# Kernel optimization log

Measured on AMD Instinct MI355X. Metric: run time of the kernel, lower is better.

Reference implementation:

```python
import jax, jax.numpy as jnp
import numpy as np

B, N, IN_DIM, OUT_DIM = 8, 2048, 128, 128
NEG_SLOPE = 0.2

def setup_inputs() -> dict:
    key = jax.random.key(0)
    k1, k2, k3, k4 = jax.random.split(key, 4)
    x = jax.random.normal(k1, (B, N, IN_DIM), dtype=jnp.float32)
    adj = jax.random.randint(k2, (N, N), 0, 2, dtype=jnp.int32)
    # nn.Linear weight init scale ~ 1/sqrt(fan_in)
    W = jax.random.normal(k3, (IN_DIM, OUT_DIM), dtype=jnp.float32) / np.sqrt(IN_DIM)
    a_vec = jax.random.normal(k4, (2 * OUT_DIM,), dtype=jnp.float32) / np.sqrt(2 * OUT_DIM)
    return {"x": x, "adj": adj, "W": W, "a_vec": a_vec}

def reference(x, adj, W, a_vec):
    # h = x @ W : [b, n, d]
    h = jnp.einsum("bni,io->bno", x, W)
    # Algebraic decomposition of a([h_i, h_j]) = a1.h_i + a2.h_j
    a1, a2 = a_vec[:OUT_DIM], a_vec[OUT_DIM:]
    s_i = h @ a1  # [b, n] score contribution from source node i
    s_j = h @ a2  # [b, n] score contribution from target node j
    e = s_i[:, :, None] + s_j[:, None, :]  # [b, n, n]
    e = jnp.where(e >= 0, e, NEG_SLOPE * e)  # leaky_relu(0.2)
    mask = (adj > 0)[None, :, :]  # [1, n, n] broadcast over batch
    e = jnp.where(mask, e, -jnp.inf)
    alpha = jax.nn.softmax(e, axis=-1)  # [b, n, n]
    out = jnp.einsum("bnm,bmd->bnd", alpha, h)  # [b, n, d]
    return out, alpha
```

## Files before the change

kernel.cpp:

```cpp
#include <hip/hip_runtime.h>
#include <hip/hip_bf16.h>
#include <cstdint>
#include <cstddef>

constexpr int Bn = 8;
constexpr int Nn = 2048;
constexpr int Dn = 128;

typedef __bf16 bf16x8 __attribute__((ext_vector_type(8)));
typedef float f32x4 __attribute__((ext_vector_type(4)));

__global__ __launch_bounds__(256) void gat_k1(
    const float* __restrict__ x, const float* __restrict__ W,
    const float* __restrict__ a_vec,
    __bf16* __restrict__ hT, float* __restrict__ s1, float* __restrict__ s2) {
  __shared__ __align__(16) float Wl[64 * 132];
  __shared__ __align__(16) float xT[64 * 68];
  __shared__ float sred[2][4][64];

  const int t = threadIdx.x;
  const int r0 = blockIdx.x * 64;
  const int b = r0 >> 11;
  const int n0 = r0 & (Nn - 1);
  const int rows = (t & 15) << 2;
  const int cols = (t >> 4) << 3;

  float acc[4][8];
#pragma unroll
  for (int r = 0; r < 4; ++r)
#pragma unroll
    for (int c = 0; c < 8; ++c) acc[r][c] = 0.f;

  for (int ph = 0; ph < 2; ++ph) {
    const int k0 = ph << 6;
    __syncthreads();
#pragma unroll
    for (int it = 0; it < 8; ++it) {
      int idx = t + (it << 8);
      int kk = idx >> 5;
      int c4 = (idx & 31) << 2;
      float4 v = *(const float4*)(W + (size_t)(k0 + kk) * Dn + c4);
      *(float4*)(Wl + kk * 132 + c4) = v;
    }
#pragma unroll
    for (int it = 0; it < 4; ++it) {
      int idx = t + (it << 8);
      int r = idx >> 4;
      int kc = (idx & 15) << 2;
      float4 v = *(const float4*)(x + (size_t)(r0 + r) * Dn + k0 + kc);
      xT[(kc + 0) * 68 + r] = v.x;
      xT[(kc + 1) * 68 + r] = v.y;
      xT[(kc + 2) * 68 + r] = v.z;
      xT[(kc + 3) * 68 + r] = v.w;
    }
    __syncthreads();
    for (int k = 0; k < 64; ++k) {
      float4 xv = *(const float4*)(xT + k * 68 + rows);
      float4 w0 = *(const float4*)(Wl + k * 132 + cols);
      float4 w1 = *(const float4*)(Wl + k * 132 + cols + 4);
      float xs[4] = {xv.x, xv.y, xv.z, xv.w};
      float ws[8] = {w0.x, w0.y, w0.z, w0.w, w1.x, w1.y, w1.z, w1.w};
#pragma unroll
      for (int r = 0; r < 4; ++r)
#pragma unroll
        for (int c = 0; c < 8; ++c) acc[r][c] = fmaf(xs[r], ws[c], acc[r][c]);
    }
  }

  float a1v[8], a2v[8];
#pragma unroll
  for (int c = 0; c < 8; ++c) {
    a1v[c] = a_vec[cols + c];
    a2v[c] = a_vec[Dn + cols + c];
  }
  const int w = t >> 6;
  const int lane = t & 63;
#pragma unroll
  for (int r = 0; r < 4; ++r) {
    float q1 = 0.f, q2 = 0.f;
#pragma unroll
    for (int c = 0; c < 8; ++c) {
      q1 = fmaf(acc[r][c], a1v[c], q1);
      q2 = fmaf(acc[r][c], a2v[c], q2);
    }
    q1 += __shfl_xor(q1, 16);
    q1 += __shfl_xor(q1, 32);
    q2 += __shfl_xor(q2, 16);
    q2 += __shfl_xor(q2, 32);
    if (lane < 16) {
      sred[0][w][rows + r] = q1;
      sred[1][w][rows + r] = q2;
    }
  }
  __syncthreads();
  if (t < 64) {
    float v1 = sred[0][0][t] + sred[0][1][t] + sred[0][2][t] + sred[0][3][t];
    float v2 = sred[1][0][t] + sred[1][1][t] + sred[1][2][t] + sred[1][3][t];
    s1[b * Nn + n0 + t] = v1;
    s2[b * Nn + n0 + t] = v2;
  }
#pragma unroll
  for (int c = 0; c < 8; ++c) {
    union { __bf16 h[4]; uint2 u; } pk;
#pragma unroll
    for (int r = 0; r < 4; ++r) pk.h[r] = (__bf16)acc[r][c];
    *(uint2*)(hT + (size_t)(b * Dn + cols + c) * Nn + n0 + rows) = pk.u;
  }
}

__global__ __launch_bounds__(256) void gat_k2(
    const int* __restrict__ adj, const __bf16* __restrict__ hT,
    const float* __restrict__ s1, const float* __restrict__ s2,
    float* __restrict__ out, float* __restrict__ alpha) {
  __shared__ __align__(16) float sj[Nn];
  __shared__ float siv_s[32];
  __shared__ float invl_s[32];
  __shared__ __align__(16) __bf16 Pl[32 * 72];
  __shared__ __align__(16) __bf16 hl[128 * 72];

  const int t = threadIdx.x;
  const int b = blockIdx.x >> 6;
  const int i0 = (blockIdx.x & 63) << 5;

  {
    const float* s2b = s2 + b * Nn;
#pragma unroll
    for (int it = 0; it < 2; ++it) {
      int idx = (t + (it << 8)) << 2;
      *(float4*)(sj + idx) = *(const float4*)(s2b + idx);
    }
    if (t < 32) siv_s[t] = s1[b * Nn + i0 + t];
  }
  __syncthreads();

  const int ii = t >> 3, sub = t & 7;
  const int i = i0 + ii;
  const int* __restrict__ adjrow = adj + (size_t)i * Nn;
  const float si = siv_s[ii];

  float l = 0.f;
  for (int cc = 0; cc < 16; ++cc) {
    int j0 = (sub + (cc << 3)) << 4;
    int4 a0 = *(const int4*)(adjrow + j0);
    int4 a1 = *(const int4*)(adjrow + j0 + 4);
    int4 a2 = *(const int4*)(adjrow + j0 + 8);
    int4 a3 = *(const int4*)(adjrow + j0 + 12);
    int m[16] = {a0.x, a0.y, a0.z, a0.w, a1.x, a1.y, a1.z, a1.w,
                 a2.x, a2.y, a2.z, a2.w, a3.x, a3.y, a3.z, a3.w};
#pragma unroll
    for (int q = 0; q < 16; ++q) {
      float e = si + sj[j0 + q];
      e = fmaxf(e, 0.2f * e);
      float ex = __expf(e);
      l += (m[q] > 0) ? ex : 0.f;
    }
  }
  l += __shfl_xor(l, 1);
  l += __shfl_xor(l, 2);
  l += __shfl_xor(l, 4);
  if (sub == 0) invl_s[ii] = 1.f / l;
  __syncthreads();
  const float il = invl_s[ii];

  const int lane = t & 63, w = t >> 6;
  const int iw = (w & 1) << 4;
  const int nb0 = (w >> 1) << 6;
  const int q16 = lane >> 4, m16 = lane & 15;
  f32x4 acc[4];
#pragma unroll
  for (int nb = 0; nb < 4; ++nb)
#pragma unroll
    for (int r = 0; r < 4; ++r) acc[nb][r] = 0.f;

  const __bf16* __restrict__ hTb = hT + (size_t)b * Dn * Nn;
  float* __restrict__ arow = alpha + ((size_t)(b * Nn + i) << 11);

  for (int jt = 0; jt < 32; ++jt) {
    const int j0 = jt << 6;
#pragma unroll
    for (int it = 0; it < 4; ++it) {
      int idx = t + (it << 8);
      int row = idx >> 3;
      int c8 = (idx & 7) << 3;
      uint4 v = *(const uint4*)(hTb + (size_t)row * Nn + j0 + c8);
      *(uint4*)(hl + row * 72 + c8) = v;
    }
    {
      int jj = sub << 3;
      int j = j0 + jj;
      int4 a0 = *(const int4*)(adjrow + j);
      int4 a1 = *(const int4*)(adjrow + j + 4);
      int m[8] = {a0.x, a0.y, a0.z, a0.w, a1.x, a1.y, a1.z, a1.w};
      float av[8];
#pragma unroll
      for (int qq = 0; qq < 8; ++qq) {
        float e = si + sj[j + qq];
        e = fmaxf(e, 0.2f * e);
        float al = __expf(e) * il;
        av[qq] = (m[qq] > 0) ? al : 0.f;
      }
      float4 f0 = make_float4(av[0], av[1], av[2], av[3]);
      float4 f1 = make_float4(av[4], av[5], av[6], av[7]);
      *(float4*)(arow + j) = f0;
      *(float4*)(arow + j + 4) = f1;
      union { __bf16 h[8]; uint4 u; } pk;
#pragma unroll
      for (int qq = 0; qq < 8; ++qq) pk.h[qq] = (__bf16)av[qq];
      *(uint4*)(Pl + ii * 72 + jj) = pk.u;
    }
    __syncthreads();
#pragma unroll
    for (int ks = 0; ks < 2; ++ks) {
      bf16x8 af = *(const bf16x8*)(Pl + (iw + m16) * 72 + (ks << 5) + (q16 << 3));
#pragma unroll
      for (int nb = 0; nb < 4; ++nb) {
        bf16x8 bf = *(const bf16x8*)(hl + (nb0 + (nb << 4) + m16) * 72 + (ks << 5) + (q16 << 3));
        acc[nb] = __builtin_amdgcn_mfma_f32_16x16x32_bf16(af, bf, acc[nb], 0, 0, 0);
      }
    }
    __syncthreads();
  }
#pragma unroll
  for (int nb = 0; nb < 4; ++nb) {
    int d = nb0 + (nb << 4) + m16;
#pragma unroll
    for (int r = 0; r < 4; ++r) {
      int irow = i0 + iw + (q16 << 2) + r;
      out[((size_t)(b * Nn + irow) << 7) + d] = acc[nb][r];
    }
  }
}

extern "C" void kernel_launch(void* const* d_in, const int* in_sizes, int n_in,
                              void* d_out, int out_size, void* d_ws, size_t ws_size,
                              hipStream_t stream) {
  const float* x = (const float*)d_in[0];
  const int* adj = (const int*)d_in[1];
  const float* W = (const float*)d_in[2];
  const float* a_vec = (const float*)d_in[3];

  float* out = (float*)d_out;
  float* alpha = out + (size_t)Bn * Nn * Dn;

  char* ws = (char*)d_ws;
  __bf16* hT = (__bf16*)ws;
  float* s1 = (float*)(ws + (size_t)Bn * Dn * Nn * 2);
  float* s2 = s1 + (size_t)Bn * Nn;

  gat_k1<<<256, 256, 0, stream>>>(x, W, a_vec, hT, s1, s2);
  gat_k2<<<512, 256, 0, stream>>>(adj, hT, s1, s2, out, alpha);
}
```

Before: 228.3 us.

## Double-buffer hT tiles via direct global-to-LDS loads and retile both kernels

The aggregation kernel now prefetches the next hT tile with global_load_lds into a second, XOR-swizzled LDS buffer, so that load can overlap the current tile's softmax and MFMA work. Double-buffering P lets each iteration use one barrier instead of two. The block grows to 512 threads and each wave computes two 16-wide output tiles, and the row-sum pass is reorganised. The projection kernel is retiled to 32 rows per block with padded W in LDS and a shuffle-only score reduction. The risk is that the async LDS loads depend on the barrier also waiting for their completion, and the larger blocks may change occupancy.

```diff
diff --git a/kernel.cpp b/kernel.cpp
--- a/kernel.cpp
+++ b/kernel.cpp
@@ -10,223 +10,213 @@
 typedef __bf16 bf16x8 __attribute__((ext_vector_type(8)));
 typedef float f32x4 __attribute__((ext_vector_type(4)));
 
+#define AS1 __attribute__((address_space(1)))
+#define AS3 __attribute__((address_space(3)))
+
+static __device__ __forceinline__ void gl_lds16(const void* g, void* l) {
+  __builtin_amdgcn_global_load_lds((AS1 const void*)g, (AS3 void*)l, 16, 0, 0);
+}
+
 __global__ __launch_bounds__(256) void gat_k1(
     const float* __restrict__ x, const float* __restrict__ W,
     const float* __restrict__ a_vec,
     __bf16* __restrict__ hT, float* __restrict__ s1, float* __restrict__ s2) {
-  __shared__ __align__(16) float Wl[64 * 132];
-  __shared__ __align__(16) float xT[64 * 68];
-  __shared__ float sred[2][4][64];
+  __shared__ __align__(16) float Wl[64 * 144];
+  __shared__ __align__(16) float xL[32 * 132];
 
   const int t = threadIdx.x;
-  const int r0 = blockIdx.x * 64;
+  const int r0 = blockIdx.x * 32;
   const int b = r0 >> 11;
   const int n0 = r0 & (Nn - 1);
-  const int rows = (t & 15) << 2;
-  const int cols = (t >> 4) << 3;
-
-  float acc[4][8];
-#pragma unroll
-  for (int r = 0; r < 4; ++r)
+  const int rp = (t >> 4) << 1;
+  const int c0 = (t & 15) << 3;
+  const int c0p = c0 + ((c0 >> 5) << 2);
+
+  float acc[2][8];
+#pragma unroll
+  for (int r = 0; r < 2; ++r)
 #pragma unroll
     for (int c = 0; c < 8; ++c) acc[r][c] = 0.f;
 
+#pragma unroll
+  for (int it = 0; it < 4; ++it) {
+    int idx = t + (it << 8);
+    int rr = idx >> 5, kc = (idx & 31) << 2;
+    *(float4*)(xL + rr * 132 + kc) = *(const float4*)(x + (size_t)(r0 + rr) * Dn + kc);
+  }
+
   for (int ph = 0; ph < 2; ++ph) {
-    const int k0 = ph << 6;
-    __syncthreads();
+    if (ph) __syncthreads();
 #pragma unroll
     for (int it = 0; it < 8; ++it) {
       int idx = t + (it << 8);
-      int kk = idx >> 5;
-      int c4 = (idx & 31) << 2;
-      float4 v = *(const float4*)(W + (size_t)(k0 + kk) * Dn + c4);
-      *(float4*)(Wl + kk * 132 + c4) = v;
-    }
-#pragma unroll
-    for (int it = 0; it < 4; ++it) {
-      int idx = t + (it << 8);
-      int r = idx >> 4;
-      int kc = (idx & 15) << 2;
-      float4 v = *(const float4*)(x + (size_t)(r0 + r) * Dn + k0 + kc);
-      xT[(kc + 0) * 68 + r] = v.x;
-      xT[(kc + 1) * 68 + r] = v.y;
-      xT[(kc + 2) * 68 + r] = v.z;
-      xT[(kc + 3) * 68 + r] = v.w;
+      int kk = idx >> 5, c4 = (idx & 31) << 2;
+      int dsto = kk * 144 + c4 + ((c4 >> 5) << 2);
+      *(float4*)(Wl + dsto) = *(const float4*)(W + (size_t)((ph << 6) + kk) * Dn + c4);
     }
     __syncthreads();
+    const float* xrow = xL + rp * 132 + (ph << 6);
     for (int k = 0; k < 64; ++k) {
-      float4 xv = *(const float4*)(xT + k * 68 + rows);
-      float4 w0 = *(const float4*)(Wl + k * 132 + cols);
-      float4 w1 = *(const float4*)(Wl + k * 132 + cols + 4);
-      float xs[4] = {xv.x, xv.y, xv.z, xv.w};
+      float xa0 = xrow[k];
+      float xa1 = xrow[132 + k];
+      float4 w0 = *(const float4*)(Wl + k * 144 + c0p);
+      float4 w1 = *(const float4*)(Wl + k * 144 + c0p + 4);
       float ws[8] = {w0.x, w0.y, w0.z, w0.w, w1.x, w1.y, w1.z, w1.w};
 #pragma unroll
-      for (int r = 0; r < 4; ++r)
-#pragma unroll
-        for (int c = 0; c < 8; ++c) acc[r][c] = fmaf(xs[r], ws[c], acc[r][c]);
-    }
-  }
-
-  float a1v[8], a2v[8];
+      for (int c = 0; c < 8; ++c) {
+        acc[0][c] = fmaf(xa0, ws[c], acc[0][c]);
+        acc[1][c] = fmaf(xa1, ws[c], acc[1][c]);
+      }
+    }
+  }
+
+  float q1[2] = {0.f, 0.f}, q2[2] = {0.f, 0.f};
 #pragma unroll
   for (int c = 0; c < 8; ++c) {
-    a1v[c] = a_vec[cols + c];
-    a2v[c] = a_vec[Dn + cols + c];
-  }
-  const int w = t >> 6;
-  const int lane = t & 63;
-#pragma unroll
-  for (int r = 0; r < 4; ++r) {
-    float q1 = 0.f, q2 = 0.f;
-#pragma unroll
-    for (int c = 0; c < 8; ++c) {
-      q1 = fmaf(acc[r][c], a1v[c], q1);
-      q2 = fmaf(acc[r][c], a2v[c], q2);
-    }
-    q1 += __shfl_xor(q1, 16);
-    q1 += __shfl_xor(q1, 32);
-    q2 += __shfl_xor(q2, 16);
-    q2 += __shfl_xor(q2, 32);
-    if (lane < 16) {
-      sred[0][w][rows + r] = q1;
-      sred[1][w][rows + r] = q2;
-    }
-  }
-  __syncthreads();
-  if (t < 64) {
-    float v1 = sred[0][0][t] + sred[0][1][t] + sred[0][2][t] + sred[0][3][t];
-    float v2 = sred[1][0][t] + sred[1][1][t] + sred[1][2][t] + sred[1][3][t];
-    s1[b * Nn + n0 + t] = v1;
-    s2[b * Nn + n0 + t] = v2;
-  }
+    float a1c = a_vec[c0 + c];
+    float a2c = a_vec[Dn + c0 + c];
+    q1[0] = fmaf(acc[0][c], a1c, q1[0]);
+    q1[1] = fmaf(acc[1][c], a1c, q1[1]);
+    q2[0] = fmaf(acc[0][c], a2c, q2[0]);
+    q2[1] = fmaf(acc[1][c], a2c, q2[1]);
+  }
+#pragma unroll
+  for (int d = 1; d < 16; d <<= 1) {
+    q1[0] += __shfl_xor(q1[0], d);
+    q1[1] += __shfl_xor(q1[1], d);
+    q2[0] += __shfl_xor(q2[0], d);
+    q2[1] += __shfl_xor(q2[1], d);
+  }
+  if ((t & 15) == 0) {
+    s1[b * Nn + n0 + rp] = q1[0];
+    s1[b * Nn + n0 + rp + 1] = q1[1];
+    s2[b * Nn + n0 + rp] = q2[0];
+    s2[b * Nn + n0 + rp + 1] = q2[1];
+  }
+
 #pragma unroll
   for (int c = 0; c < 8; ++c) {
-    union { __bf16 h[4]; uint2 u; } pk;
-#pragma unroll
-    for (int r = 0; r < 4; ++r) pk.h[r] = (__bf16)acc[r][c];
-    *(uint2*)(hT + (size_t)(b * Dn + cols + c) * Nn + n0 + rows) = pk.u;
-  }
-}
-
-__global__ __launch_bounds__(256) void gat_k2(
+    union { __bf16 h[2]; uint32_t u; } pk;
+    pk.h[0] = (__bf16)acc[0][c];
+    pk.h[1] = (__bf16)acc[1][c];
+    *(uint32_t*)(hT + (size_t)(b * Dn + c0 + c) * Nn + n0 + rp) = pk.u;
+  }
+}
+
+__global__ __launch_bounds__(512) void gat_k2(
     const int* __restrict__ adj, const __bf16* __restrict__ hT,
     const float* __restrict__ s1, const float* __restrict__ s2,
     float* __restrict__ out, float* __restrict__ alpha) {
   __shared__ __align__(16) float sj[Nn];
-  __shared__ float siv_s[32];
-  __shared__ float invl_s[32];
-  __shared__ __align__(16) __bf16 Pl[32 * 72];
-  __shared__ __align__(16) __bf16 hl[128 * 72];
+  __shared__ float siv[32], invl[32];
+  __shared__ __align__(16) __bf16 Pl[2][32 * 72];
+  __shared__ __align__(16) __bf16 hl[2][128 * 64];
 
   const int t = threadIdx.x;
   const int b = blockIdx.x >> 6;
   const int i0 = (blockIdx.x & 63) << 5;
-
-  {
-    const float* s2b = s2 + b * Nn;
-#pragma unroll
-    for (int it = 0; it < 2; ++it) {
-      int idx = (t + (it << 8)) << 2;
-      *(float4*)(sj + idx) = *(const float4*)(s2b + idx);
-    }
-    if (t < 32) siv_s[t] = s1[b * Nn + i0 + t];
-  }
+  const int w = t >> 6, lane = t & 63;
+  const int ii = t >> 4, sub = t & 15;
+  const int lrow = lane >> 3, ccs = lane & 7;
+  const __bf16* __restrict__ hTb = hT + (size_t)b * Dn * Nn;
+
+#pragma unroll
+  for (int inst = 0; inst < 2; ++inst) {
+    int row = (w << 4) + (inst << 3) + lrow;
+    gl_lds16(hTb + (size_t)row * Nn + ((ccs ^ lrow) << 3),
+             &hl[0][((w << 4) + (inst << 3)) << 6]);
+  }
+
+  *(float4*)(sj + (t << 2)) = *(const float4*)(s2 + b * Nn + (t << 2));
+  if (t < 32) siv[t] = s1[b * Nn + i0 + t];
   __syncthreads();
 
-  const int ii = t >> 3, sub = t & 7;
   const int i = i0 + ii;
   const int* __restrict__ adjrow = adj + (size_t)i * Nn;
-  const float si = siv_s[ii];
+  const float si = siv[ii];
 
   float l = 0.f;
-  for (int cc = 0; cc < 16; ++cc) {
-    int j0 = (sub + (cc << 3)) << 4;
-    int4 a0 = *(const int4*)(adjrow + j0);
-    int4 a1 = *(const int4*)(adjrow + j0 + 4);
-    int4 a2 = *(const int4*)(adjrow + j0 + 8);
-    int4 a3 = *(const int4*)(adjrow + j0 + 12);
-    int m[16] = {a0.x, a0.y, a0.z, a0.w, a1.x, a1.y, a1.z, a1.w,
-                 a2.x, a2.y, a2.z, a2.w, a3.x, a3.y, a3.z, a3.w};
-#pragma unroll
-    for (int q = 0; q < 16; ++q) {
-      float e = si + sj[j0 + q];
-      e = fmaxf(e, 0.2f * e);
-      float ex = __expf(e);
-      l += (m[q] > 0) ? ex : 0.f;
-    }
+  for (int cc = 0; cc < 32; ++cc) {
+    int j = (cc << 6) + (sub << 2);
+    int4 am = *(const int4*)(adjrow + j);
+    float4 sv = *(const float4*)(sj + j);
+    float e;
+    e = si + sv.x; e = fmaxf(e, 0.2f * e); l += (am.x > 0) ? __expf(e) : 0.f;
+    e = si + sv.y; e = fmaxf(e, 0.2f * e); l += (am.y > 0) ? __expf(e) : 0.f;
+    e = si + sv.z; e = fmaxf(e, 0.2f * e); l += (am.z > 0) ? __expf(e) : 0.f;
+    e = si + sv.w; e = fmaxf(e, 0.2f * e); l += (am.w > 0) ? __expf(e) : 0.f;
   }
   l += __shfl_xor(l, 1);
   l += __shfl_xor(l, 2);
   l += __shfl_xor(l, 4);
-  if (sub == 0) invl_s[ii] = 1.f / l;
+  l += __shfl_xor(l, 8);
+  if (sub == 0) invl[ii] = 1.f / l;
   __syncthreads();
-  const float il = invl_s[ii];
-
-  const int lane = t & 63, w = t >> 6;
+  const float il = invl[ii];
+
   const int iw = (w & 1) << 4;
-  const int nb0 = (w >> 1) << 6;
+  const int nd0 = (w >> 1) << 5;
   const int q16 = lane >> 4, m16 = lane & 15;
-  f32x4 acc[4];
-#pragma unroll
-  for (int nb = 0; nb < 4; ++nb)
-#pragma unroll
-    for (int r = 0; r < 4; ++r) acc[nb][r] = 0.f;
-
-  const __bf16* __restrict__ hTb = hT + (size_t)b * Dn * Nn;
+  f32x4 acc0 = {0.f, 0.f, 0.f, 0.f}, acc1 = {0.f, 0.f, 0.f, 0.f};
   float* __restrict__ arow = alpha + ((size_t)(b * Nn + i) << 11);
 
   for (int jt = 0; jt < 32; ++jt) {
+    const int buf = jt & 1;
     const int j0 = jt << 6;
-#pragma unroll
-    for (int it = 0; it < 4; ++it) {
-      int idx = t + (it << 8);
-      int row = idx >> 3;
-      int c8 = (idx & 7) << 3;
-      uint4 v = *(const uint4*)(hTb + (size_t)row * Nn + j0 + c8);
-      *(uint4*)(hl + row * 72 + c8) = v;
-    }
     {
-      int jj = sub << 3;
-      int j = j0 + jj;
-      int4 a0 = *(const int4*)(adjrow + j);
-      int4 a1 = *(const int4*)(adjrow + j + 4);
-      int m[8] = {a0.x, a0.y, a0.z, a0.w, a1.x, a1.y, a1.z, a1.w};
-      float av[8];
-#pragma unroll
-      for (int qq = 0; qq < 8; ++qq) {
-        float e = si + sj[j + qq];
-        e = fmaxf(e, 0.2f * e);
-        float al = __expf(e) * il;
-        av[qq] = (m[qq] > 0) ? al : 0.f;
-      }
-      float4 f0 = make_float4(av[0], av[1], av[2], av[3]);
-      float4 f1 = make_float4(av[4], av[5], av[6], av[7]);
-      *(float4*)(arow + j) = f0;
-      *(float4*)(arow + j + 4) = f1;
-      union { __bf16 h[8]; uint4 u; } pk;
-#pragma unroll
-      for (int qq = 0; qq < 8; ++qq) pk.h[qq] = (__bf16)av[qq];
-      *(uint4*)(Pl + ii * 72 + jj) = pk.u;
+      int j = j0 + (sub << 2);
+      int4 am = *(const int4*)(adjrow + j);
+      float4 sv = *(const float4*)(sj + j);
+      float e0 = si + sv.x; e0 = fmaxf(e0, 0.2f * e0);
+      float e1 = si + sv.y; e1 = fmaxf(e1, 0.2f * e1);
+      float e2 = si + sv.z; e2 = fmaxf(e2, 0.2f * e2);
+      float e3 = si + sv.w; e3 = fmaxf(e3, 0.2f * e3);
+      float a0 = (am.x > 0) ? __expf(e0) * il : 0.f;
+      float a1 = (am.y > 0) ? __expf(e1) * il : 0.f;
+      float a2 = (am.z > 0) ? __expf(e2) * il : 0.f;
+      float a3 = (am.w > 0) ? __expf(e3) * il : 0.f;
+      *(float4*)(arow + j) = make_float4(a0, a1, a2, a3);
+      union { __bf16 h[4]; uint2 u; } pk;
+      pk.h[0] = (__bf16)a0; pk.h[1] = (__bf16)a1;
+      pk.h[2] = (__bf16)a2; pk.h[3] = (__bf16)a3;
+      *(uint2*)(&Pl[buf][ii * 72 + (sub << 2)]) = pk.u;
     }
     __syncthreads();
+    if (jt < 31) {
+      int jn = j0 + 64;
+#pragma unroll
+      for (int inst = 0; inst < 2; ++inst) {
+        int row = (w << 4) + (inst << 3) + lrow;
+        gl_lds16(hTb + (size_t)row * Nn + jn + ((ccs ^ lrow) << 3),
+                 &hl[buf ^ 1][((w << 4) + (inst << 3)) << 6]);
+      }
+    }
 #pragma unroll
     for (int ks = 0; ks < 2; ++ks) {
-      bf16x8 af = *(const bf16x8*)(Pl + (iw + m16) * 72 + (ks << 5) + (q16 << 3));
-#pragma unroll
-      for (int nb = 0; nb < 4; ++nb) {
-        bf16x8 bf = *(const bf16x8*)(hl + (nb0 + (nb << 4) + m16) * 72 + (ks << 5) + (q16 << 3));
-        acc[nb] = __builtin_amdgcn_mfma_f32_16x16x32_bf16(af, bf, acc[nb], 0, 0, 0);
-      }
-    }
-    __syncthreads();
-  }
-#pragma unroll
-  for (int nb = 0; nb < 4; ++nb) {
-    int d = nb0 + (nb << 4) + m16;
+      bf16x8 af = *(const bf16x8*)(&Pl[buf][(iw + m16) * 72 + (ks << 5) + (q16 << 3)]);
+      {
+        int d = nd0 + m16;
+        int phys = ((ks << 2) + q16) ^ (d & 7);
+        bf16x8 bv = *(const bf16x8*)(&hl[buf][(d << 6) + (phys << 3)]);
+        acc0 = __builtin_amdgcn_mfma_f32_16x16x32_bf16(af, bv, acc0, 0, 0, 0);
+      }
+      {
+        int d = nd0 + 16 + m16;
+        int phys = ((ks << 2) + q16) ^ (d & 7);
+        bf16x8 bv = *(const bf16x8*)(&hl[buf][(d << 6) + (phys << 3)]);
+        acc1 = __builtin_amdgcn_mfma_f32_16x16x32_bf16(af, bv, acc1, 0, 0, 0);
+      }
+    }
+  }
+
+#pragma unroll
+  for (int nb = 0; nb < 2; ++nb) {
+    f32x4 a = nb ? acc1 : acc0;
+    int d = nd0 + (nb << 4) + m16;
 #pragma unroll
     for (int r = 0; r < 4; ++r) {
       int irow = i0 + iw + (q16 << 2) + r;
-      out[((size_t)(b * Nn + irow) << 7) + d] = acc[nb][r];
+      out[((size_t)(b * Nn + irow) << 7) + d] = a[r];
     }
   }
 }
@@ -247,6 +237,6 @@
   float* s1 = (float*)(ws + (size_t)Bn * Dn * Nn * 2);
   float* s2 = s1 + (size_t)Bn * Nn;
 
-  gat_k1<<<256, 256, 0, stream>>>(x, W, a_vec, hT, s1, s2);
-  gat_k2<<<512, 256, 0, stream>>>(adj, hT, s1, s2, out, alpha);
-}
+  gat_k1<<<512, 256, 0, stream>>>(x, W, a_vec, hT, s1, s2);
+  gat_k2<<<512, 512, 0, stream>>>(adj, hT, s1, s2, out, alpha);
+}
```

Result: faster. 194.1 us (-15.0%).
